# Optimization experiments

Measured on AMD Instinct MI355X. Metric: run time of the kernel, lower is better.

## Reference

```python
import jax, jax.numpy as jnp
import numpy as np

N_NODES = 100000
N_EDGES = 1600000
D_IN, D_HID, D_OUT = 512, 256, 32


def setup_inputs() -> dict:
    key = jax.random.key(0)
    ks = jax.random.split(key, 8)
    features = jax.random.normal(ks[0], (N_NODES, D_IN), dtype=jnp.float32)
    A_data = jax.random.uniform(ks[1], (N_EDGES,), dtype=jnp.float32)
    A_row = jax.random.randint(ks[2], (N_EDGES,), 0, N_NODES, dtype=jnp.int32)
    A_col = jax.random.randint(ks[3], (N_EDGES,), 0, N_NODES, dtype=jnp.int32)
    # MLP params (glorot-ish scaling)
    W1 = jax.random.normal(ks[4], (D_IN, D_HID), dtype=jnp.float32) * (1.0 / np.sqrt(D_IN))
    b1 = jnp.zeros((D_HID,), dtype=jnp.float32)
    W2 = jax.random.normal(ks[5], (D_HID, D_OUT), dtype=jnp.float32) * (1.0 / np.sqrt(D_HID))
    b2 = jnp.zeros((D_OUT,), dtype=jnp.float32)
    return {"features": features, "A_data": A_data, "W1": W1, "b1": b1,
            "W2": W2, "b2": b2, "A_row": A_row, "A_col": A_col}


def reference(features, A_data, W1, b1, W2, b2, A_row, A_col):
    # head_transform: 2-layer MLP (is_training=False -> dropout identity)
    h = jax.nn.relu(features @ W1 + b1)          # [N, D_HID]
    X = h @ W2 + b2                              # [N, D_OUT]
    # propagator dropout: rate=0.0 / eval mode -> identity on A
    # sparse COO A @ X: gather columns, scale by edge values, scatter-add to rows
    msgs = A_data[:, None] * X[A_col]            # [E, D_OUT]
    out = jax.ops.segment_sum(msgs, A_row, num_segments=N_NODES)  # [N, D_OUT]
    return out
```

## Files before the change

### kernel.cpp

```cpp
#include <hip/hip_runtime.h>
#include <hip/hip_bf16.h>

typedef __bf16 bf16;
typedef __attribute__((ext_vector_type(8))) __bf16 bf16x8;
typedef __attribute__((ext_vector_type(4))) float f32x4;

constexpr int D_IN  = 512;
constexpr int D_HID = 256;
constexpr int D_OUT = 32;
constexpr int BM = 64;
constexpr int BK = 32;
constexpr int HPAD = 264;
constexpr int SCAN_VPT  = 8;
constexpr int SCAN_SPAN = 2048;

__global__ __launch_bounds__(256) void prep_kernel(
    const float* __restrict__ W1, const float* __restrict__ W2,
    bf16* __restrict__ W1T, bf16* __restrict__ W2T)
{
    int idx = blockIdx.x * 256 + threadIdx.x;
    if (idx < D_IN * D_HID) {
        int k = idx / D_HID, n = idx % D_HID;
        W1T[n * D_IN + k] = (bf16)W1[idx];
    }
    int j = idx - D_IN * D_HID;
    if (j >= 0 && j < D_HID * D_OUT) {
        int k = j / D_OUT, n = j % D_OUT;
        W2T[n * D_HID + k] = (bf16)W2[j];
    }
}

__global__ __launch_bounds__(256) void fused_mlp_kernel(
    const float* __restrict__ feat,
    const bf16* __restrict__ W1T, const bf16* __restrict__ W2T,
    const float* __restrict__ b1, const float* __restrict__ b2,
    float* __restrict__ X, int N)
{
    __shared__ __align__(16) bf16 Asm[BM * BK];
    __shared__ __align__(16) bf16 Bsm[D_HID * BK];
    __shared__ __align__(16) bf16 Hsm[BM * HPAD];
    __shared__ __align__(16) bf16 B2sm[D_OUT * HPAD];

    const int tid  = threadIdx.x;
    const int wave = tid >> 6;
    const int lane = tid & 63;
    const int ln   = lane & 15;
    const int q    = lane >> 4;
    const int mw   = wave * 16;
    const int r0   = blockIdx.x * BM;

    #pragma unroll
    for (int i = 0; i < 4; ++i) {
        int c  = tid + i * 256;
        int n  = c >> 5;
        int kc = (c & 31) * 8;
        *(bf16x8*)&B2sm[n * HPAD + kc] = *(const bf16x8*)&W2T[n * D_HID + kc];
    }

    f32x4 acc[16] = {};

    const int am   = tid >> 2;
    const int asub = (tid & 3) * 8;
    const long arow = (long)min(r0 + am, N - 1);
    const float* asrc = feat + arow * D_IN + asub;

    for (int k0 = 0; k0 < D_IN; k0 += BK) {
        float4 f0 = *(const float4*)(asrc + k0);
        float4 f1 = *(const float4*)(asrc + k0 + 4);
        bf16x8 av;
        av[0] = (bf16)f0.x; av[1] = (bf16)f0.y; av[2] = (bf16)f0.z; av[3] = (bf16)f0.w;
        av[4] = (bf16)f1.x; av[5] = (bf16)f1.y; av[6] = (bf16)f1.z; av[7] = (bf16)f1.w;
        *(bf16x8*)&Asm[am * BK + asub] = av;

        #pragma unroll
        for (int i = 0; i < 4; ++i) {
            int c   = tid + i * 256;
            int n   = c >> 2;
            int kc8 = (c & 3) * 8;
            *(bf16x8*)&Bsm[n * BK + kc8] =
                *(const bf16x8*)&W1T[n * D_IN + k0 + kc8];
        }
        __syncthreads();

        bf16x8 af = *(const bf16x8*)&Asm[(mw + ln) * BK + q * 8];
        #pragma unroll
        for (int t = 0; t < 16; ++t) {
            bf16x8 bf = *(const bf16x8*)&Bsm[(t * 16 + ln) * BK + q * 8];
            acc[t] = __builtin_amdgcn_mfma_f32_16x16x32_bf16(af, bf, acc[t], 0, 0, 0);
        }
        __syncthreads();
    }

    #pragma unroll
    for (int t = 0; t < 16; ++t) {
        int colh = t * 16 + ln;
        float bb = b1[colh];
        #pragma unroll
        for (int i = 0; i < 4; ++i) {
            int row = mw + q * 4 + i;
            float v = acc[t][i] + bb;
            Hsm[row * HPAD + colh] = (bf16)fmaxf(v, 0.0f);
        }
    }
    __syncthreads();

    f32x4 acc2[2] = {};
    #pragma unroll
    for (int k0 = 0; k0 < D_HID; k0 += BK) {
        bf16x8 af = *(const bf16x8*)&Hsm[(mw + ln) * HPAD + k0 + q * 8];
        #pragma unroll
        for (int t = 0; t < 2; ++t) {
            bf16x8 bf = *(const bf16x8*)&B2sm[(t * 16 + ln) * HPAD + k0 + q * 8];
            acc2[t] = __builtin_amdgcn_mfma_f32_16x16x32_bf16(af, bf, acc2[t], 0, 0, 0);
        }
    }

    #pragma unroll
    for (int t = 0; t < 2; ++t) {
        int c = t * 16 + ln;
        float bb = b2[c];
        #pragma unroll
        for (int i = 0; i < 4; ++i) {
            int row = r0 + mw + q * 4 + i;
            if (row < N) X[row * D_OUT + c] = acc2[t][i] + bb;
        }
    }
}

__global__ __launch_bounds__(256) void hist_kernel(
    const int* __restrict__ Arow, int* __restrict__ counts, int E)
{
    int e = blockIdx.x * 256 + threadIdx.x;
    if (e < E) atomicAdd(&counts[Arow[e]], 1);
}

__global__ __launch_bounds__(256) void scanA_kernel(
    const int* __restrict__ counts, int* __restrict__ offs,
    int* __restrict__ partials, int N)
{
    __shared__ int lds[256];
    int t = threadIdx.x;
    int base = blockIdx.x * SCAN_SPAN + t * SCAN_VPT;
    int v[SCAN_VPT];
    int tsum = 0;
    #pragma unroll
    for (int j = 0; j < SCAN_VPT; ++j) {
        v[j] = (base + j < N) ? counts[base + j] : 0;
        tsum += v[j];
    }
    lds[t] = tsum;
    __syncthreads();
    for (int d = 1; d < 256; d <<= 1) {
        int x = (t >= d) ? lds[t - d] : 0;
        __syncthreads();
        lds[t] += x;
        __syncthreads();
    }
    int run = lds[t] - tsum;
    #pragma unroll
    for (int j = 0; j < SCAN_VPT; ++j) {
        if (base + j < N) offs[base + j] = run;
        run += v[j];
    }
    if (t == 255) partials[blockIdx.x] = lds[255];
}

__global__ __launch_bounds__(256) void scanB_kernel(int* __restrict__ partials, int nb)
{
    __shared__ int lds[256];
    int t = threadIdx.x;
    int v = (t < nb) ? partials[t] : 0;
    lds[t] = v;
    __syncthreads();
    for (int d = 1; d < 256; d <<= 1) {
        int x = (t >= d) ? lds[t - d] : 0;
        __syncthreads();
        lds[t] += x;
        __syncthreads();
    }
    if (t < nb) partials[t] = lds[t] - v;
}

__global__ __launch_bounds__(256) void scanC_kernel(
    int* __restrict__ offs, const int* __restrict__ partials,
    int* __restrict__ cursor, int N)
{
    int i = blockIdx.x * 256 + threadIdx.x;
    if (i < N) {
        int o = offs[i] + partials[i / SCAN_SPAN];
        offs[i] = o;
        cursor[i] = o;
    }
}

__global__ __launch_bounds__(256) void reorder_kernel(
    const int* __restrict__ Arow, const int* __restrict__ Acol,
    const float* __restrict__ Adata, int* __restrict__ cursor,
    int* __restrict__ col_s, float* __restrict__ a_s, int E)
{
    int e = blockIdx.x * 256 + threadIdx.x;
    if (e >= E) return;
    int r = Arow[e];
    int p = atomicAdd(&cursor[r], 1);
    col_s[p] = Acol[e];
    a_s[p]   = Adata[e];
}

__global__ __launch_bounds__(256) void reduce_kernel(
    const int* __restrict__ offs, const int* __restrict__ counts,
    const int* __restrict__ col_s, const float* __restrict__ a_s,
    const float* __restrict__ X, float* __restrict__ out, int N)
{
    int w    = threadIdx.x >> 6;
    int lane = threadIdx.x & 63;
    int r    = blockIdx.x * 4 + w;
    if (r >= N) return;
    int half = lane >> 5;
    int dim  = lane & 31;
    int off  = offs[r];
    int deg  = counts[r];
    float acc = 0.0f;
    int i = half;
    for (; i + 2 < deg; i += 4) {
        int   c0 = col_s[off + i];
        float a0 = a_s[off + i];
        int   c1 = col_s[off + i + 2];
        float a1 = a_s[off + i + 2];
        acc += a0 * X[(long)c0 * D_OUT + dim];
        acc += a1 * X[(long)c1 * D_OUT + dim];
    }
    for (; i < deg; i += 2) {
        int   c = col_s[off + i];
        float a = a_s[off + i];
        acc += a * X[(long)c * D_OUT + dim];
    }
    acc += __shfl_xor(acc, 32, 64);
    if (!half) out[(long)r * D_OUT + dim] = acc;
}

__global__ __launch_bounds__(256) void scatter_kernel(
    const float* __restrict__ Adata, const int* __restrict__ Arow,
    const int* __restrict__ Acol, const float* __restrict__ X,
    float* __restrict__ out, int E)
{
    int idx = blockIdx.x * 256 + threadIdx.x;
    int e = idx >> 3;
    int g = idx & 7;
    if (e >= E) return;
    int   col = Acol[e];
    int   row = Arow[e];
    float a   = Adata[e];
    float4 x = *(const float4*)(X + (long)col * D_OUT + g * 4);
    float* o = out + (long)row * D_OUT + g * 4;
    unsafeAtomicAdd(o + 0, a * x.x);
    unsafeAtomicAdd(o + 1, a * x.y);
    unsafeAtomicAdd(o + 2, a * x.z);
    unsafeAtomicAdd(o + 3, a * x.w);
}

extern "C" void kernel_launch(void* const* d_in, const int* in_sizes, int n_in,
                              void* d_out, int out_size, void* d_ws, size_t ws_size,
                              hipStream_t stream)
{
    const float* feat  = (const float*)d_in[0];
    const float* Adata = (const float*)d_in[1];
    const float* W1    = (const float*)d_in[2];
    const float* b1    = (const float*)d_in[3];
    const float* W2    = (const float*)d_in[4];
    const float* b2    = (const float*)d_in[5];
    const int*   Arow  = (const int*)d_in[6];
    const int*   Acol  = (const int*)d_in[7];

    const int N = in_sizes[0] / D_IN;
    const int E = in_sizes[1];

    char* p = (char*)d_ws;
    auto alloc = [&](size_t bytes) {
        char* q = p;
        p += (bytes + 255) & ~(size_t)255;
        return q;
    };
    float* X       = (float*)alloc((size_t)N * D_OUT * sizeof(float));
    bf16*  W1T     = (bf16*) alloc((size_t)D_IN * D_HID * sizeof(bf16));
    bf16*  W2T     = (bf16*) alloc((size_t)D_HID * D_OUT * sizeof(bf16));
    int*   counts  = (int*)  alloc((size_t)N * sizeof(int));
    int*   offs    = (int*)  alloc((size_t)N * sizeof(int));
    int*   cursor  = (int*)  alloc((size_t)N * sizeof(int));
    int*   partials= (int*)  alloc(256 * sizeof(int));
    int*   col_s   = (int*)  alloc((size_t)E * sizeof(int));
    float* a_s     = (float*)alloc((size_t)E * sizeof(float));
    size_t need = (size_t)(p - (char*)d_ws);
    const bool use_csr = (need <= ws_size);

    float* out = (float*)d_out;

    int prep_elems = D_IN * D_HID + D_HID * D_OUT;
    prep_kernel<<<(prep_elems + 255) / 256, 256, 0, stream>>>(W1, W2, W1T, W2T);

    fused_mlp_kernel<<<(N + BM - 1) / BM, 256, 0, stream>>>(
        feat, W1T, W2T, b1, b2, X, N);

    if (use_csr) {
        hipMemsetAsync(counts, 0, (size_t)N * sizeof(int), stream);
        hist_kernel<<<(E + 255) / 256, 256, 0, stream>>>(Arow, counts, E);
        int nb = (N + SCAN_SPAN - 1) / SCAN_SPAN;
        scanA_kernel<<<nb, 256, 0, stream>>>(counts, offs, partials, N);
        scanB_kernel<<<1, 256, 0, stream>>>(partials, nb);
        scanC_kernel<<<(N + 255) / 256, 256, 0, stream>>>(offs, partials, cursor, N);
        reorder_kernel<<<(E + 255) / 256, 256, 0, stream>>>(
            Arow, Acol, Adata, cursor, col_s, a_s, E);
        reduce_kernel<<<(N + 3) / 4, 256, 0, stream>>>(
            offs, counts, col_s, a_s, X, out, N);
    } else {
        hipMemsetAsync(out, 0, (size_t)out_size * sizeof(float), stream);
        long scatter_threads = (long)E * 8;
        scatter_kernel<<<(scatter_threads + 255) / 256, 256, 0, stream>>>(
            Adata, Arow, Acol, X, out, E);
    }
}
```

Baseline: 576.2 us.

## Use direct global-to-LDS loads for W1, alias LDS buffers, pack CSR pairs, vectorize reduce

The MLP kernel now streams W1T tiles into LDS with global_load_lds instead of going through registers. It also aliases the A/B staging buffers with the H buffer to shrink LDS use, which may raise occupancy, and changes HPAD padding. The CSR path packs column index and edge value into one int2 so each edge needs a single load. The reduce kernel now has 8 edge slots per wave, each lane loading float4 of X, followed by a shuffle reduction. These changes risk LDS bank conflicts from the new padding and hazards from the buffer aliasing, which depend on sync placement.

```diff
diff --git a/kernel.cpp b/kernel.cpp
--- a/kernel.cpp
+++ b/kernel.cpp
@@ -10,9 +10,12 @@
 constexpr int D_OUT = 32;
 constexpr int BM = 64;
 constexpr int BK = 32;
-constexpr int HPAD = 264;
+constexpr int HPAD = 260;
 constexpr int SCAN_VPT  = 8;
 constexpr int SCAN_SPAN = 2048;
+
+#define GLOBAL_AS(p) ((const __attribute__((address_space(1))) void*)(p))
+#define LDS_AS(p)    ((__attribute__((address_space(3))) void*)(p))
 
 __global__ __launch_bounds__(256) void prep_kernel(
     const float* __restrict__ W1, const float* __restrict__ W2,
@@ -36,10 +39,11 @@
     const float* __restrict__ b1, const float* __restrict__ b2,
     float* __restrict__ X, int N)
 {
-    __shared__ __align__(16) bf16 Asm[BM * BK];
-    __shared__ __align__(16) bf16 Bsm[D_HID * BK];
-    __shared__ __align__(16) bf16 Hsm[BM * HPAD];
-    __shared__ __align__(16) bf16 B2sm[D_OUT * HPAD];
+    __shared__ __align__(16) char smem[(BM + D_OUT) * HPAD * sizeof(bf16)];
+    bf16* Asm  = (bf16*)smem;
+    bf16* Bsm  = (bf16*)(smem + BM * BK * 2);
+    bf16* Hsm  = (bf16*)smem;
+    bf16* B2sm = (bf16*)(smem + BM * HPAD * 2);
 
     const int tid  = threadIdx.x;
     const int wave = tid >> 6;
@@ -65,6 +69,14 @@
     const float* asrc = feat + arow * D_IN + asub;
 
     for (int k0 = 0; k0 < D_IN; k0 += BK) {
+        #pragma unroll
+        for (int i = 0; i < 4; ++i) {
+            int c = i * 256 + wave * 64 + lane;
+            const bf16* gsrc = W1T + ((c >> 2) * D_IN + k0 + (c & 3) * 8);
+            bf16* lbase = Bsm + (i * 256 + wave * 64) * 8;
+            __builtin_amdgcn_global_load_lds(GLOBAL_AS(gsrc), LDS_AS(lbase), 16, 0, 0);
+        }
+
         float4 f0 = *(const float4*)(asrc + k0);
         float4 f1 = *(const float4*)(asrc + k0 + 4);
         bf16x8 av;
@@ -72,14 +84,6 @@
         av[4] = (bf16)f1.x; av[5] = (bf16)f1.y; av[6] = (bf16)f1.z; av[7] = (bf16)f1.w;
         *(bf16x8*)&Asm[am * BK + asub] = av;
 
-        #pragma unroll
-        for (int i = 0; i < 4; ++i) {
-            int c   = tid + i * 256;
-            int n   = c >> 2;
-            int kc8 = (c & 3) * 8;
-            *(bf16x8*)&Bsm[n * BK + kc8] =
-                *(const bf16x8*)&W1T[n * D_IN + k0 + kc8];
-        }
         __syncthreads();
 
         bf16x8 af = *(const bf16x8*)&Asm[(mw + ln) * BK + q * 8];
@@ -196,46 +200,46 @@
 __global__ __launch_bounds__(256) void reorder_kernel(
     const int* __restrict__ Arow, const int* __restrict__ Acol,
     const float* __restrict__ Adata, int* __restrict__ cursor,
-    int* __restrict__ col_s, float* __restrict__ a_s, int E)
+    int2* __restrict__ pairs, int E)
 {
     int e = blockIdx.x * 256 + threadIdx.x;
     if (e >= E) return;
     int r = Arow[e];
     int p = atomicAdd(&cursor[r], 1);
-    col_s[p] = Acol[e];
-    a_s[p]   = Adata[e];
+    int2 pk;
+    pk.x = Acol[e];
+    pk.y = __float_as_int(Adata[e]);
+    pairs[p] = pk;
 }
 
 __global__ __launch_bounds__(256) void reduce_kernel(
     const int* __restrict__ offs, const int* __restrict__ counts,
-    const int* __restrict__ col_s, const float* __restrict__ a_s,
-    const float* __restrict__ X, float* __restrict__ out, int N)
+    const int2* __restrict__ pairs, const float* __restrict__ X,
+    float* __restrict__ out, int N)
 {
     int w    = threadIdx.x >> 6;
     int lane = threadIdx.x & 63;
     int r    = blockIdx.x * 4 + w;
     if (r >= N) return;
-    int half = lane >> 5;
-    int dim  = lane & 31;
+    int slot = lane >> 3;
+    int dg   = lane & 7;
     int off  = offs[r];
     int deg  = counts[r];
-    float acc = 0.0f;
-    int i = half;
-    for (; i + 2 < deg; i += 4) {
-        int   c0 = col_s[off + i];
-        float a0 = a_s[off + i];
-        int   c1 = col_s[off + i + 2];
-        float a1 = a_s[off + i + 2];
-        acc += a0 * X[(long)c0 * D_OUT + dim];
-        acc += a1 * X[(long)c1 * D_OUT + dim];
-    }
-    for (; i < deg; i += 2) {
-        int   c = col_s[off + i];
-        float a = a_s[off + i];
-        acc += a * X[(long)c * D_OUT + dim];
-    }
-    acc += __shfl_xor(acc, 32, 64);
-    if (!half) out[(long)r * D_OUT + dim] = acc;
+    f32x4 acc = {0.0f, 0.0f, 0.0f, 0.0f};
+    for (int i = slot; i < deg; i += 8) {
+        int2  pk = pairs[off + i];
+        float a  = __int_as_float(pk.y);
+        f32x4 x  = *(const f32x4*)(X + (long)pk.x * D_OUT + dg * 4);
+        acc += a * x;
+    }
+    #pragma unroll
+    for (int d = 8; d < 64; d <<= 1) {
+        acc[0] += __shfl_xor(acc[0], d, 64);
+        acc[1] += __shfl_xor(acc[1], d, 64);
+        acc[2] += __shfl_xor(acc[2], d, 64);
+        acc[3] += __shfl_xor(acc[3], d, 64);
+    }
+    if (slot == 0) *(f32x4*)(out + (long)r * D_OUT + dg * 4) = acc;
 }
 
 __global__ __launch_bounds__(256) void scatter_kernel(
@@ -287,8 +291,7 @@
     int*   offs    = (int*)  alloc((size_t)N * sizeof(int));
     int*   cursor  = (int*)  alloc((size_t)N * sizeof(int));
     int*   partials= (int*)  alloc(256 * sizeof(int));
-    int*   col_s   = (int*)  alloc((size_t)E * sizeof(int));
-    float* a_s     = (float*)alloc((size_t)E * sizeof(float));
+    int2*  pairs   = (int2*) alloc((size_t)E * sizeof(int2));
     size_t need = (size_t)(p - (char*)d_ws);
     const bool use_csr = (need <= ws_size);
 
@@ -308,9 +311,9 @@
         scanB_kernel<<<1, 256, 0, stream>>>(partials, nb);
         scanC_kernel<<<(N + 255) / 256, 256, 0, stream>>>(offs, partials, cursor, N);
         reorder_kernel<<<(E + 255) / 256, 256, 0, stream>>>(
-            Arow, Acol, Adata, cursor, col_s, a_s, E);
+            Arow, Acol, Adata, cursor, pairs, E);
         reduce_kernel<<<(N + 3) / 4, 256, 0, stream>>>(
-            offs, counts, col_s, a_s, X, out, N);
+            offs, counts, pairs, X, out, N);
     } else {
         hipMemsetAsync(out, 0, (size_t)out_size * sizeof(float), stream);
         long scatter_threads = (long)E * 8;
```

After: 574.6 us. About the same (-0.3%).
